# Kernel tuning notes

Hardware: AMD Instinct MI355X
Metric: run time of the kernel (lower is better)

The kernel has to match this reference:

```python
import jax, jax.numpy as jnp
import numpy as np

B, L, H, D = 4, 2048, 8, 64

def setup_inputs() -> dict:
    key = jax.random.key(0)
    kq, kk, kv = jax.random.split(key, 3)
    return {
        "queries": jax.random.normal(kq, (B, L, H, D), dtype=jnp.float32),
        "keys": jax.random.normal(kk, (B, L, H, D), dtype=jnp.float32),
        "values": jax.random.normal(kv, (B, L, H, D), dtype=jnp.float32),
    }

def reference(queries, keys, values):
    # QK^T over head_dim: [m,q,w,h]
    QK = jnp.einsum('mqhd,mwhd->mqwh', queries, keys)
    softmax_temp = 1.0 / jnp.sqrt(jnp.asarray(queries.shape[3], QK.dtype))
    A = jax.nn.softmax(softmax_temp * QK, axis=2)
    # Faithful to source: values einsum uses index 'e' (summed independently),
    # reproducing the original module's exact math.
    out = jnp.einsum('mqwh,mehd->mqhd', A, values)
    return out
```

## Files before the change

kernel.cpp:

```cpp
#include <hip/hip_runtime.h>


#define Bm     4
#define Lseq   2048
#define HD     512
#define C4     128
#define NCHUNK 128
#define CH_E   (Lseq / NCHUNK)
#define PART_FLOATS (Bm * NCHUNK * HD)

__global__ void vsum_partial(const float4* __restrict__ v4,
                             float4* __restrict__ part4) {
    const int m   = blockIdx.x / NCHUNK;
    const int ch  = blockIdx.x % NCHUNK;
    const int t   = threadIdx.x;
    const int c4  = t & (C4 - 1);
    const int sub = t >> 7;

    const float4* base =
        v4 + (size_t)(m * Lseq + ch * CH_E + sub * (CH_E / 2)) * C4 + c4;

    float4 acc = make_float4(0.f, 0.f, 0.f, 0.f);
#pragma unroll
    for (int i = 0; i < CH_E / 2; ++i) {
        float4 x = base[(size_t)i * C4];
        acc.x += x.x; acc.y += x.y; acc.z += x.z; acc.w += x.w;
    }

    __shared__ float4 red[C4];
    if (sub) red[c4] = acc;
    __syncthreads();
    if (!sub) {
        float4 o = red[c4];
        acc.x += o.x; acc.y += o.y; acc.z += o.z; acc.w += o.w;
        part4[(size_t)blockIdx.x * C4 + c4] = acc;
    }
}

__global__ void vsum_final(const float* __restrict__ part,
                           float* __restrict__ vsum) {
    const int j   = blockIdx.x * blockDim.x + threadIdx.x;
    const int m   = j >> 9;
    const int col = j & (HD - 1);
    const float* p = part + (size_t)m * NCHUNK * HD + col;
    float s = 0.f;
#pragma unroll 8
    for (int ch = 0; ch < NCHUNK; ++ch) s += p[(size_t)ch * HD];
    vsum[j] = s;
}

__global__ void vsum_broadcast(const float4* __restrict__ vsum4,
                               float4* __restrict__ out4) {
    const int idx = blockIdx.x * blockDim.x + threadIdx.x;
    const int c4  = idx & (C4 - 1);
    const int m   = idx >> 18;
    out4[idx] = vsum4[m * C4 + c4];
}

extern "C" void kernel_launch(void* const* d_in, const int* in_sizes, int n_in,
                              void* d_out, int out_size, void* d_ws, size_t ws_size,
                              hipStream_t stream) {
    const float* values = (const float*)d_in[2];
    float*       part   = (float*)d_ws;
    float*       vsum   = (float*)d_ws + PART_FLOATS;
    float*       out    = (float*)d_out;

    vsum_partial<<<Bm * NCHUNK, 256, 0, stream>>>((const float4*)values,
                                                  (float4*)part);

    vsum_final<<<(Bm * HD) / 256, 256, 0, stream>>>(part, vsum);

    const int total4 = Bm * Lseq * C4;
    vsum_broadcast<<<total4 / 256, 256, 0, stream>>>((const float4*)vsum,
                                                     (float4*)out);
}
```

Measured before the change: 94.69 us.

## Fuse column-sum and broadcast into a single kernel with redundant per-block reduction

Replaces the three-kernel partial-sum, final-sum and broadcast pipeline with one kernel. Each block reduces a column slice of V over the full sequence in registers and shared memory, then writes that slice to a quarter of the output rows. This removes two launches and the workspace round trip, at the cost of reading V four times and running only 256 blocks with long serial load loops.

```diff
diff --git a/kernel.cpp b/kernel.cpp
--- a/kernel.cpp
+++ b/kernel.cpp
@@ -3,74 +3,58 @@
 
 #define Bm     4
 #define Lseq   2048
-#define HD     512
 #define C4     128
-#define NCHUNK 128
-#define CH_E   (Lseq / NCHUNK)
-#define PART_FLOATS (Bm * NCHUNK * HD)
+#define SW     8
+#define SLICES (C4 / SW)
+#define QCH    4
+#define QROWS  (Lseq / QCH)
 
-__global__ void vsum_partial(const float4* __restrict__ v4,
-                             float4* __restrict__ part4) {
-    const int m   = blockIdx.x / NCHUNK;
-    const int ch  = blockIdx.x % NCHUNK;
-    const int t   = threadIdx.x;
-    const int c4  = t & (C4 - 1);
-    const int sub = t >> 7;
+__global__ __launch_bounds__(256)
+void fused_sum_bcast(const float4* __restrict__ v4, float4* __restrict__ out4) {
+    const int b  = blockIdx.x;
+    const int j  = b >> 6;
+    const int r  = b & 63;
+    const int m  = r >> 4;
+    const int s0 = (r & (SLICES - 1)) * SW;
 
-    const float4* base =
-        v4 + (size_t)(m * Lseq + ch * CH_E + sub * (CH_E / 2)) * C4 + c4;
+    const int t  = threadIdx.x;
+    const int ct = t & (SW - 1);
+    const int rt = t >> 3;
+
+    const float4* vp = v4 + ((size_t)m * Lseq + rt) * C4 + s0 + ct;
 
     float4 acc = make_float4(0.f, 0.f, 0.f, 0.f);
-#pragma unroll
-    for (int i = 0; i < CH_E / 2; ++i) {
-        float4 x = base[(size_t)i * C4];
+#pragma unroll 8
+    for (int i = 0; i < Lseq / 32; ++i) {
+        float4 x = vp[(size_t)i * 32 * C4];
         acc.x += x.x; acc.y += x.y; acc.z += x.z; acc.w += x.w;
     }
 
-    __shared__ float4 red[C4];
-    if (sub) red[c4] = acc;
+    __shared__ float4 red[32][SW];
+    red[rt][ct] = acc;
     __syncthreads();
-    if (!sub) {
-        float4 o = red[c4];
-        acc.x += o.x; acc.y += o.y; acc.z += o.z; acc.w += o.w;
-        part4[(size_t)blockIdx.x * C4 + c4] = acc;
+#pragma unroll
+    for (int s = 16; s >= 1; s >>= 1) {
+        if (rt < s) {
+            float4 a = red[rt][ct], o = red[rt + s][ct];
+            a.x += o.x; a.y += o.y; a.z += o.z; a.w += o.w;
+            red[rt][ct] = a;
+        }
+        __syncthreads();
     }
-}
+    const float4 vs = red[0][ct];
 
-__global__ void vsum_final(const float* __restrict__ part,
-                           float* __restrict__ vsum) {
-    const int j   = blockIdx.x * blockDim.x + threadIdx.x;
-    const int m   = j >> 9;
-    const int col = j & (HD - 1);
-    const float* p = part + (size_t)m * NCHUNK * HD + col;
-    float s = 0.f;
-#pragma unroll 8
-    for (int ch = 0; ch < NCHUNK; ++ch) s += p[(size_t)ch * HD];
-    vsum[j] = s;
-}
-
-__global__ void vsum_broadcast(const float4* __restrict__ vsum4,
-                               float4* __restrict__ out4) {
-    const int idx = blockIdx.x * blockDim.x + threadIdx.x;
-    const int c4  = idx & (C4 - 1);
-    const int m   = idx >> 18;
-    out4[idx] = vsum4[m * C4 + c4];
+    float4* op = out4 + ((size_t)m * Lseq + j * QROWS + rt) * C4 + s0 + ct;
+#pragma unroll
+    for (int i = 0; i < QROWS / 32; ++i) {
+        op[(size_t)i * 32 * C4] = vs;
+    }
 }
 
 extern "C" void kernel_launch(void* const* d_in, const int* in_sizes, int n_in,
                               void* d_out, int out_size, void* d_ws, size_t ws_size,
                               hipStream_t stream) {
-    const float* values = (const float*)d_in[2];
-    float*       part   = (float*)d_ws;
-    float*       vsum   = (float*)d_ws + PART_FLOATS;
-    float*       out    = (float*)d_out;
-
-    vsum_partial<<<Bm * NCHUNK, 256, 0, stream>>>((const float4*)values,
-                                                  (float4*)part);
-
-    vsum_final<<<(Bm * HD) / 256, 256, 0, stream>>>(part, vsum);
-
-    const int total4 = Bm * Lseq * C4;
-    vsum_broadcast<<<total4 / 256, 256, 0, stream>>>((const float4*)vsum,
-                                                     (float4*)out);
+    (void)in_sizes; (void)n_in; (void)d_ws; (void)ws_size; (void)out_size;
+    const float4* values = (const float4*)d_in[2];
+    fused_sum_bcast<<<Bm * SLICES * QCH, 256, 0, stream>>>(values, (float4*)d_out);
 }
```

Result: faster. 88.38 us (-6.7%).
